# Kernel tuning notes

Measured on AMD Instinct MI355X. Metric: run time of the kernel, lower is better.

The kernel has to match this reference:

```python
import jax, jax.numpy as jnp
import numpy as np

N = 100000
K = 20
SCALES = (5, 10, 20)
D = 256  # dimoffeat


def _leaky(x):
    return jax.nn.leaky_relu(x, negative_slope=0.2)


def setup_inputs() -> dict:
    key = jax.random.key(0)
    ks = jax.random.split(key, 20)
    S = len(SCALES)
    inp = {
        "points": jax.random.normal(ks[0], (N, 3), dtype=jnp.float32),
        "neighbor_indices": jax.random.randint(ks[1], (N, K), 0, N, dtype=jnp.int64),
        # per-scale patch PointNet weights, stacked over the 3 scales
        "pw1": jax.random.normal(ks[2], (S, D // 4, 3), dtype=jnp.float32) * 0.05,
        "pb1": jax.random.normal(ks[3], (S, D // 4), dtype=jnp.float32) * 0.05,
        "pw2": jax.random.normal(ks[4], (S, D // 2, D // 4), dtype=jnp.float32) * 0.05,
        "pb2": jax.random.normal(ks[5], (S, D // 2), dtype=jnp.float32) * 0.05,
        "pw3": jax.random.normal(ks[6], (S, D, D // 2), dtype=jnp.float32) * 0.05,
        "pb3": jax.random.normal(ks[7], (S, D), dtype=jnp.float32) * 0.05,
        # shared MLP (all 1x1 convs == linears)
        "sw1": jax.random.normal(ks[8], (D, S * D), dtype=jnp.float32) * 0.05,
        "sb1": jax.random.normal(ks[9], (D,), dtype=jnp.float32) * 0.05,
        "sw2": jax.random.normal(ks[10], (D // 2, D), dtype=jnp.float32) * 0.05,
        "sb2": jax.random.normal(ks[11], (D // 2,), dtype=jnp.float32) * 0.05,
        "sw3": jax.random.normal(ks[12], (D // 4, D // 2), dtype=jnp.float32) * 0.05,
        "sb3": jax.random.normal(ks[13], (D // 4,), dtype=jnp.float32) * 0.05,
        "sw4": jax.random.normal(ks[14], (D // 8, D // 4), dtype=jnp.float32) * 0.05,
        "sb4": jax.random.normal(ks[15], (D // 8,), dtype=jnp.float32) * 0.05,
        "sw5": jax.random.normal(ks[16], (1, D // 8), dtype=jnp.float32) * 0.05,
        "sb5": jax.random.normal(ks[17], (1,), dtype=jnp.float32) * 0.05,
    }
    return inp


def reference(points, pw1, pb1, pw2, pb2, pw3, pb3,
              sw1, sb1, sw2, sb2, sw3, sb3, sw4, sb4, sw5, sb5,
              neighbor_indices):
    feats_list = []
    for i, s in enumerate(SCALES):
        # gather neighbors and center: [N, s, 3]
        nb = points[neighbor_indices[:, :s]] - points[:, None, :]
        # 1x1-conv MLP == per-point linear layers
        h = _leaky(jnp.einsum('nsc,dc->nsd', nb, pw1[i]) + pb1[i])
        h = _leaky(jnp.einsum('nsc,dc->nsd', h, pw2[i]) + pb2[i])
        h = jnp.einsum('nsc,dc->nsd', h, pw3[i]) + pb3[i]
        feats_list.append(jnp.max(h, axis=1))  # max-pool over neighbors -> [N, D]
    x = jnp.concatenate(feats_list, axis=1)  # [N, 3*D]
    h = _leaky(x @ sw1.T + sb1)
    h = _leaky(h @ sw2.T + sb2)
    h = _leaky(h @ sw3.T + sb3)
    h = _leaky(h @ sw4.T + sb4)
    out = h @ sw5.T + sb5  # [N, 1]
    return out[:, 0]
```

## Files before the change

### kernel.cpp

```cpp
#include <hip/hip_runtime.h>


typedef _Float16 f16x8 __attribute__((ext_vector_type(8)));
typedef float f32x4 __attribute__((ext_vector_type(4)));

#define NPTS 100000
#define PPB 32
#define KMAX 20

#define PW2OFF 0
#define PW3OFF 24576
#define SW1OFF 122880
#define SW2OFF 319488
#define SW3OFF 352256
#define SW4OFF 360448
#define NFRAGS 708
#define PW1PAD_BYTES 724992

__device__ __forceinline__ float leaky(float x) { return fmaxf(x, 0.2f * x); }

struct PrepRegion { const float* src; int inC; int Kk; int fEnd; int dstOff; };
struct PrepParams {
    PrepRegion r[10];
    const float* pw1; const float* pb1;
    float* pw1pad; _Float16* dst;
};

__global__ __launch_bounds__(256) void prep_kernel(PrepParams pp) {
    int gid = blockIdx.x * 256 + threadIdx.x;
    if (gid < NFRAGS * 64) {
        int f = gid >> 6, L = gid & 63;
        int ri = 0;
        while (f >= pp.r[ri].fEnd) ri++;
        int f0 = (ri == 0) ? 0 : pp.r[ri - 1].fEnd;
        const PrepRegion R = pp.r[ri];
        int fl = f - f0;
        int nt = fl / R.Kk, kk = fl - nt * R.Kk;
        int row = nt * 16 + (L & 15);
        int col = kk * 32 + (L >> 4) * 8;
        const float* s = R.src + row * R.inC + col;
        f16x8 v;
#pragma unroll
        for (int j = 0; j < 8; ++j) v[j] = (_Float16)s[j];
        *(f16x8*)(pp.dst + R.dstOff + fl * 512 + L * 8) = v;
    } else if (gid < NFRAGS * 64 + 192) {
        int t = gid - NFRAGS * 64;
        int i = t >> 6, fd = t & 63;
        float4 w;
        w.x = pp.pw1[i * 192 + fd * 3 + 0];
        w.y = pp.pw1[i * 192 + fd * 3 + 1];
        w.z = pp.pw1[i * 192 + fd * 3 + 2];
        w.w = pp.pb1[i * 64 + fd];
        ((float4*)pp.pw1pad)[i * 64 + fd] = w;
    }
}

struct MainParams {
    const float* points; const int* nidx;
    const float* pb2; const float* pb3;
    const float* sb1; const float* sb2; const float* sb3; const float* sb4;
    const float* sw5; const float* sb5;
    const _Float16* wsH; const float* pw1pad;
    float* out;
    int n;
};

#define LDS_BYTES 41472

__global__ __launch_bounds__(256, 2) void msp_mfma(MainParams p) {
    __shared__ __align__(16) unsigned char pool[LDS_BYTES];
    float*     nbf  = (float*)pool;
    float*     pw1s = (float*)(pool + 10240);
    _Float16*  h1   = (_Float16*)(pool + 11264);
    _Float16*  h2   = (_Float16*)(pool + 15872);
    _Float16*  xi   = (_Float16*)(pool + 24576);

    const int tid  = threadIdx.x;
    const int wave = tid >> 6, lane = tid & 63;
    const int q = lane >> 4, m16 = lane & 15;
    const int n0 = blockIdx.x * PPB;

    for (int r = tid; r < PPB * KMAX; r += 256) {
        int pp_ = r & 31, k = r >> 5;
        int idx = p.nidx[(n0 + pp_) * KMAX + k];
        const float* npt = p.points + idx * 3;
        const float* cpt = p.points + (n0 + pp_) * 3;
        float4 v;
        v.x = npt[0] - cpt[0];
        v.y = npt[1] - cpt[1];
        v.z = npt[2] - cpt[2];
        v.w = 1.0f;
        ((float4*)nbf)[r] = v;
    }

    f32x4 accC[2][4];
#pragma unroll
    for (int mt = 0; mt < 2; ++mt)
#pragma unroll
        for (int t = 0; t < 4; ++t) accC[mt][t] = (f32x4){0.f, 0.f, 0.f, 0.f};

    __syncthreads();

    const int SS[3] = {5, 10, 20};
    for (int i = 0; i < 3; ++i) {
        const int S = SS[i];
        if (tid < 64)
            ((float4*)pw1s)[tid] = ((const float4*)p.pw1pad)[i * 64 + tid];

        f16x8 W2f[2][2], W3f[4][4];
#pragma unroll
        for (int t2 = 0; t2 < 2; ++t2)
#pragma unroll
            for (int kk = 0; kk < 2; ++kk)
                W2f[t2][kk] = *(const f16x8*)(p.wsH + PW2OFF +
                    (i * 16 + (2 * wave + t2) * 2 + kk) * 512 + lane * 8);
#pragma unroll
        for (int t3 = 0; t3 < 4; ++t3)
#pragma unroll
            for (int kk = 0; kk < 4; ++kk)
                W3f[t3][kk] = *(const f16x8*)(p.wsH + PW3OFF +
                    (i * 64 + (4 * wave + t3) * 4 + kk) * 512 + lane * 8);

        float b2v[2], b3v[4];
#pragma unroll
        for (int t2 = 0; t2 < 2; ++t2) b2v[t2] = p.pb2[i * 128 + (2 * wave + t2) * 16 + m16];
#pragma unroll
        for (int t3 = 0; t3 < 4; ++t3) b3v[t3] = p.pb3[i * 256 + (4 * wave + t3) * 16 + m16];

        f32x4 maxC[2][4];
#pragma unroll
        for (int mt = 0; mt < 2; ++mt)
#pragma unroll
            for (int t3 = 0; t3 < 4; ++t3)
                maxC[mt][t3] = (f32x4){-3.0e38f, -3.0e38f, -3.0e38f, -3.0e38f};

        __syncthreads();

        for (int k = 0; k < S; ++k) {
            {
                int row = tid & 31, g = tid >> 5;
                float4 nv = ((const float4*)nbf)[k * 32 + row];
                f16x8 hv;
#pragma unroll
                for (int j = 0; j < 8; ++j) {
                    float4 w = ((const float4*)pw1s)[g * 8 + j];
                    float v = fmaf(nv.x, w.x, fmaf(nv.y, w.y, fmaf(nv.z, w.z, w.w)));
                    hv[j] = (_Float16)leaky(v);
                }
                *(f16x8*)(h1 + row * 72 + g * 8) = hv;
            }
            __syncthreads();

#pragma unroll
            for (int mt = 0; mt < 2; ++mt) {
                const _Float16* ar = h1 + (mt * 16 + m16) * 72 + q * 8;
                f16x8 a0 = *(const f16x8*)(ar);
                f16x8 a1 = *(const f16x8*)(ar + 32);
                f32x4 acc[2];
#pragma unroll
                for (int t2 = 0; t2 < 2; ++t2) {
                    acc[t2] = __builtin_amdgcn_mfma_f32_16x16x32_f16(a0, W2f[t2][0],
                              (f32x4){0.f, 0.f, 0.f, 0.f}, 0, 0, 0);
                }
#pragma unroll
                for (int t2 = 0; t2 < 2; ++t2)
                    acc[t2] = __builtin_amdgcn_mfma_f32_16x16x32_f16(a1, W2f[t2][1], acc[t2], 0, 0, 0);
#pragma unroll
                for (int t2 = 0; t2 < 2; ++t2) {
                    int colb = (2 * wave + t2) * 16 + m16;
#pragma unroll
                    for (int r = 0; r < 4; ++r) {
                        float v = leaky(acc[t2][r] + b2v[t2]);
                        h2[(mt * 16 + q * 4 + r) * 136 + colb] = (_Float16)v;
                    }
                }
            }
            __syncthreads();

#pragma unroll
            for (int mt = 0; mt < 2; ++mt) {
                const _Float16* ar = h2 + (mt * 16 + m16) * 136;
                f16x8 a[4];
#pragma unroll
                for (int kk = 0; kk < 4; ++kk)
                    a[kk] = *(const f16x8*)(ar + kk * 32 + q * 8);
                f32x4 acc[4];
#pragma unroll
                for (int t3 = 0; t3 < 4; ++t3)
                    acc[t3] = __builtin_amdgcn_mfma_f32_16x16x32_f16(a[0], W3f[t3][0],
                              (f32x4){0.f, 0.f, 0.f, 0.f}, 0, 0, 0);
#pragma unroll
                for (int kk = 1; kk < 4; ++kk)
#pragma unroll
                    for (int t3 = 0; t3 < 4; ++t3)
                        acc[t3] = __builtin_amdgcn_mfma_f32_16x16x32_f16(a[kk], W3f[t3][kk], acc[t3], 0, 0, 0);
#pragma unroll
                for (int t3 = 0; t3 < 4; ++t3)
#pragma unroll
                    for (int r = 0; r < 4; ++r)
                        maxC[mt][t3][r] = fmaxf(maxC[mt][t3][r], acc[t3][r]);
            }
        }

#pragma unroll
        for (int mt = 0; mt < 2; ++mt)
#pragma unroll
            for (int t3 = 0; t3 < 4; ++t3) {
                int col = (4 * wave + t3) * 16 + m16;
#pragma unroll
                for (int r = 0; r < 4; ++r)
                    xi[(mt * 16 + q * 4 + r) * 264 + col] = (_Float16)(maxC[mt][t3][r] + b3v[t3]);
            }
        __syncthreads();

#pragma unroll
        for (int mt = 0; mt < 2; ++mt) {
            const _Float16* ar = xi + (mt * 16 + m16) * 264;
            f16x8 a[8];
#pragma unroll
            for (int kk = 0; kk < 8; ++kk)
                a[kk] = *(const f16x8*)(ar + kk * 32 + q * 8);
#pragma unroll
            for (int kk = 0; kk < 8; ++kk)
#pragma unroll
                for (int t = 0; t < 4; ++t) {
                    int nt = 4 * wave + t;
                    f16x8 b = *(const f16x8*)(p.wsH + SW1OFF +
                        (nt * 24 + i * 8 + kk) * 512 + lane * 8);
                    accC[mt][t] = __builtin_amdgcn_mfma_f32_16x16x32_f16(a[kk], b, accC[mt][t], 0, 0, 0);
                }
        }
        __syncthreads();
    }

#pragma unroll
    for (int mt = 0; mt < 2; ++mt)
#pragma unroll
        for (int t = 0; t < 4; ++t) {
            int col = (4 * wave + t) * 16 + m16;
            float b = p.sb1[col];
#pragma unroll
            for (int r = 0; r < 4; ++r)
                xi[(mt * 16 + q * 4 + r) * 264 + col] = (_Float16)leaky(accC[mt][t][r] + b);
        }
    __syncthreads();

#pragma unroll
    for (int mt = 0; mt < 2; ++mt) {
        const _Float16* ar = xi + (mt * 16 + m16) * 264;
        f16x8 a[8];
#pragma unroll
        for (int kk = 0; kk < 8; ++kk)
            a[kk] = *(const f16x8*)(ar + kk * 32 + q * 8);
        f32x4 acc[2];
        acc[0] = acc[1] = (f32x4){0.f, 0.f, 0.f, 0.f};
#pragma unroll
        for (int kk = 0; kk < 8; ++kk)
#pragma unroll
            for (int t2 = 0; t2 < 2; ++t2) {
                int nt = 2 * wave + t2;
                f16x8 b = *(const f16x8*)(p.wsH + SW2OFF + (nt * 8 + kk) * 512 + lane * 8);
                acc[t2] = __builtin_amdgcn_mfma_f32_16x16x32_f16(a[kk], b, acc[t2], 0, 0, 0);
            }
#pragma unroll
        for (int t2 = 0; t2 < 2; ++t2) {
            int col = (2 * wave + t2) * 16 + m16;
            float b = p.sb2[col];
#pragma unroll
            for (int r = 0; r < 4; ++r)
                h2[(mt * 16 + q * 4 + r) * 136 + col] = (_Float16)leaky(acc[t2][r] + b);
        }
    }
    __syncthreads();

    {
        f16x8 a[2][4];
#pragma unroll
        for (int mt = 0; mt < 2; ++mt) {
            const _Float16* ar = h2 + (mt * 16 + m16) * 136;
#pragma unroll
            for (int kk = 0; kk < 4; ++kk)
                a[mt][kk] = *(const f16x8*)(ar + kk * 32 + q * 8);
        }
        f32x4 acc[2];
        acc[0] = acc[1] = (f32x4){0.f, 0.f, 0.f, 0.f};
#pragma unroll
        for (int kk = 0; kk < 4; ++kk) {
            f16x8 b = *(const f16x8*)(p.wsH + SW3OFF + (wave * 4 + kk) * 512 + lane * 8);
#pragma unroll
            for (int mt = 0; mt < 2; ++mt)
                acc[mt] = __builtin_amdgcn_mfma_f32_16x16x32_f16(a[mt][kk], b, acc[mt], 0, 0, 0);
        }
        int col = wave * 16 + m16;
        float bb = p.sb3[col];
#pragma unroll
        for (int mt = 0; mt < 2; ++mt)
#pragma unroll
            for (int r = 0; r < 4; ++r)
                h1[(mt * 16 + q * 4 + r) * 72 + col] = (_Float16)leaky(acc[mt][r] + bb);
    }
    __syncthreads();

    if (wave < 2) {
#pragma unroll
        for (int mt = 0; mt < 2; ++mt) {
            const _Float16* ar = h1 + (mt * 16 + m16) * 72;
            f16x8 a0 = *(const f16x8*)(ar + q * 8);
            f16x8 a1 = *(const f16x8*)(ar + 32 + q * 8);
            f32x4 acc = __builtin_amdgcn_mfma_f32_16x16x32_f16(a0,
                *(const f16x8*)(p.wsH + SW4OFF + (wave * 2 + 0) * 512 + lane * 8),
                (f32x4){0.f, 0.f, 0.f, 0.f}, 0, 0, 0);
            acc = __builtin_amdgcn_mfma_f32_16x16x32_f16(a1,
                *(const f16x8*)(p.wsH + SW4OFF + (wave * 2 + 1) * 512 + lane * 8),
                acc, 0, 0, 0);
            int col = wave * 16 + m16;
            float b = p.sb4[col];
#pragma unroll
            for (int r = 0; r < 4; ++r)
                nbf[(mt * 16 + q * 4 + r) * 33 + col] = leaky(acc[r] + b);
        }
    }
    __syncthreads();

    if (tid < PPB) {
        float acc = p.sb5[0];
#pragma unroll
        for (int c = 0; c < 32; ++c)
            acc = fmaf(nbf[tid * 33 + c], p.sw5[c], acc);
        p.out[n0 + tid] = acc;
    }
}

extern "C" void kernel_launch(void* const* d_in, const int* in_sizes, int n_in,
                              void* d_out, int out_size, void* d_ws, size_t ws_size,
                              hipStream_t stream) {
    const float* points = (const float*)d_in[0];
    const int*   nidx   = (const int*)d_in[1];
    const float* pw1 = (const float*)d_in[2];  const float* pb1 = (const float*)d_in[3];
    const float* pw2 = (const float*)d_in[4];  const float* pb2 = (const float*)d_in[5];
    const float* pw3 = (const float*)d_in[6];  const float* pb3 = (const float*)d_in[7];
    const float* sw1 = (const float*)d_in[8];  const float* sb1 = (const float*)d_in[9];
    const float* sw2 = (const float*)d_in[10]; const float* sb2 = (const float*)d_in[11];
    const float* sw3 = (const float*)d_in[12]; const float* sb3 = (const float*)d_in[13];
    const float* sw4 = (const float*)d_in[14]; const float* sb4 = (const float*)d_in[15];
    const float* sw5 = (const float*)d_in[16]; const float* sb5 = (const float*)d_in[17];

    _Float16* wsH = (_Float16*)d_ws;
    float* pw1pad = (float*)((char*)d_ws + PW1PAD_BYTES);

    PrepParams pp;
    for (int i = 0; i < 3; ++i)
        pp.r[i] = { pw2 + i * 8192, 64, 2, 16 * (i + 1), PW2OFF + i * 8192 };
    for (int i = 0; i < 3; ++i)
        pp.r[3 + i] = { pw3 + i * 32768, 128, 4, 48 + 64 * (i + 1), PW3OFF + i * 32768 };
    pp.r[6] = { sw1, 768, 24, 624, SW1OFF };
    pp.r[7] = { sw2, 256, 8, 688, SW2OFF };
    pp.r[8] = { sw3, 128, 4, 704, SW3OFF };
    pp.r[9] = { sw4, 64, 2, 708, SW4OFF };
    pp.pw1 = pw1; pp.pb1 = pb1;
    pp.pw1pad = pw1pad; pp.dst = wsH;

    int prep_threads = NFRAGS * 64 + 192;
    hipLaunchKernelGGL(prep_kernel, dim3((prep_threads + 255) / 256), dim3(256), 0, stream, pp);

    MainParams mp;
    mp.points = points; mp.nidx = nidx;
    mp.pb2 = pb2; mp.pb3 = pb3;
    mp.sb1 = sb1; mp.sb2 = sb2; mp.sb3 = sb3; mp.sb4 = sb4;
    mp.sw5 = sw5; mp.sb5 = sb5;
    mp.wsH = wsH; mp.pw1pad = pw1pad;
    mp.out = (float*)d_out;
    mp.n = in_sizes[0] / 3;

    int blocks = mp.n / PPB;
    hipLaunchKernelGGL(msp_mfma, dim3(blocks), dim3(256), 0, stream, mp);
}
```

Before: 502.2 us.

## Batch five neighbors per MFMA pass with transposed operands and folded biases

The patch-MLP loop now processes chunks of five neighbors at once (160 rows), so one barrier pair covers five neighbors instead of one and there are fewer synchronisations per scale. MFMA operands are swapped so weights are the A operand and activations the B operand, which allows packed f16x4 vector stores to LDS and bias loading as the accumulator init. Layer-1 weights move from LDS into registers, and bias plus leaky for layer 2 are done in packed half precision with round-toward-zero conversion. LDS use nearly doubles to 76.8KB, which may reduce occupancy, and the half-precision activation adds small rounding differences.

New measurement: 517.5 us. +3.1%, slower.

```diff
diff --git a/kernel.cpp b/kernel.cpp
--- a/kernel.cpp
+++ b/kernel.cpp
@@ -2,9 +2,10 @@
 
 
 typedef _Float16 f16x8 __attribute__((ext_vector_type(8)));
-typedef float f32x4 __attribute__((ext_vector_type(4)));
-
-#define NPTS 100000
+typedef _Float16 f16x4 __attribute__((ext_vector_type(4)));
+typedef __fp16   h16x2 __attribute__((ext_vector_type(2)));
+typedef float    f32x4 __attribute__((ext_vector_type(4)));
+
 #define PPB 32
 #define KMAX 20
 
@@ -17,7 +18,41 @@
 #define NFRAGS 708
 #define PW1PAD_BYTES 724992
 
-__device__ __forceinline__ float leaky(float x) { return fmaxf(x, 0.2f * x); }
+#define NB_OFF 0
+#define H1_OFF 10240
+#define H2_OFF 33280
+#define LDS_BYTES 76800
+#define H1S 72
+#define H2S 136
+#define XIS 264
+#define X2S 264
+#define H3S 136
+#define H4S 72
+#define O4S 36
+
+__device__ __forceinline__ float leakyf(float x) { return fmaxf(x, 0.2f * x); }
+
+__device__ __forceinline__ f16x4 pkrtz4(f32x4 a) {
+    h16x2 lo = __builtin_amdgcn_cvt_pkrtz(a[0], a[1]);
+    h16x2 hi = __builtin_amdgcn_cvt_pkrtz(a[2], a[3]);
+    f16x4 r;
+    r[0] = (_Float16)lo[0]; r[1] = (_Float16)lo[1];
+    r[2] = (_Float16)hi[0]; r[3] = (_Float16)hi[1];
+    return r;
+}
+__device__ __forceinline__ f16x4 leaky4h(f16x4 h) {
+    f16x4 s = h * (_Float16)0.2f;
+    return __builtin_elementwise_max(h, s);
+}
+__device__ __forceinline__ f16x4 rne4(f32x4 a) {
+    f16x4 r; r[0] = (_Float16)a[0]; r[1] = (_Float16)a[1];
+    r[2] = (_Float16)a[2]; r[3] = (_Float16)a[3];
+    return r;
+}
+__device__ __forceinline__ f32x4 ldbias4(const float* b) {
+    float4 t = *(const float4*)b;
+    return (f32x4){t.x, t.y, t.z, t.w};
+}
 
 struct PrepRegion { const float* src; int inC; int Kk; int fEnd; int dstOff; };
 struct PrepParams {
@@ -65,15 +100,16 @@
     int n;
 };
 
-#define LDS_BYTES 41472
-
 __global__ __launch_bounds__(256, 2) void msp_mfma(MainParams p) {
     __shared__ __align__(16) unsigned char pool[LDS_BYTES];
-    float*     nbf  = (float*)pool;
-    float*     pw1s = (float*)(pool + 10240);
-    _Float16*  h1   = (_Float16*)(pool + 11264);
-    _Float16*  h2   = (_Float16*)(pool + 15872);
-    _Float16*  xi   = (_Float16*)(pool + 24576);
+    float*    nbf = (float*)(pool + NB_OFF);
+    _Float16* h1  = (_Float16*)(pool + H1_OFF);
+    _Float16* h2  = (_Float16*)(pool + H2_OFF);
+    _Float16* xi  = (_Float16*)(pool + H2_OFF);
+    _Float16* x2  = (_Float16*)(pool + H1_OFF);
+    _Float16* h3  = (_Float16*)(pool + NB_OFF);
+    _Float16* h4  = (_Float16*)(pool + H2_OFF);
+    float*    out4= (float*)(pool + H2_OFF + 8192);
 
     const int tid  = threadIdx.x;
     const int wave = tid >> 6, lane = tid & 63;
@@ -95,229 +131,201 @@
 
     f32x4 accC[2][4];
 #pragma unroll
-    for (int mt = 0; mt < 2; ++mt)
-#pragma unroll
-        for (int t = 0; t < 4; ++t) accC[mt][t] = (f32x4){0.f, 0.f, 0.f, 0.f};
-
-    __syncthreads();
-
-    const int SS[3] = {5, 10, 20};
+    for (int mt = 0; mt < 4; ++mt) {
+        f32x4 b = ldbias4(p.sb1 + (wave * 4 + mt) * 16 + q * 4);
+        accC[0][mt] = b; accC[1][mt] = b;
+    }
+    __syncthreads();
+
+    const int NC[3] = {1, 2, 4};
     for (int i = 0; i < 3; ++i) {
-        const int S = SS[i];
-        if (tid < 64)
-            ((float4*)pw1s)[tid] = ((const float4*)p.pw1pad)[i * 64 + tid];
-
         f16x8 W2f[2][2], W3f[4][4];
 #pragma unroll
-        for (int t2 = 0; t2 < 2; ++t2)
+        for (int mt = 0; mt < 2; ++mt)
 #pragma unroll
             for (int kk = 0; kk < 2; ++kk)
-                W2f[t2][kk] = *(const f16x8*)(p.wsH + PW2OFF +
-                    (i * 16 + (2 * wave + t2) * 2 + kk) * 512 + lane * 8);
-#pragma unroll
-        for (int t3 = 0; t3 < 4; ++t3)
+                W2f[mt][kk] = *(const f16x8*)(p.wsH + PW2OFF +
+                    (i * 16 + (wave * 2 + mt) * 2 + kk) * 512 + lane * 8);
+#pragma unroll
+        for (int mt = 0; mt < 4; ++mt)
 #pragma unroll
             for (int kk = 0; kk < 4; ++kk)
-                W3f[t3][kk] = *(const f16x8*)(p.wsH + PW3OFF +
-                    (i * 64 + (4 * wave + t3) * 4 + kk) * 512 + lane * 8);
-
-        float b2v[2], b3v[4];
-#pragma unroll
-        for (int t2 = 0; t2 < 2; ++t2) b2v[t2] = p.pb2[i * 128 + (2 * wave + t2) * 16 + m16];
-#pragma unroll
-        for (int t3 = 0; t3 < 4; ++t3) b3v[t3] = p.pb3[i * 256 + (4 * wave + t3) * 16 + m16];
+                W3f[mt][kk] = *(const f16x8*)(p.wsH + PW3OFF +
+                    (i * 64 + (wave * 4 + mt) * 4 + kk) * 512 + lane * 8);
+
+        float4 w1r[8];
+        {
+            const float4* pw14 = (const float4*)p.pw1pad + i * 64 + (tid >> 5) * 8;
+#pragma unroll
+            for (int j = 0; j < 8; ++j) w1r[j] = pw14[j];
+        }
+        f32x4 b2v[2], b3v[4];
+#pragma unroll
+        for (int mt = 0; mt < 2; ++mt)
+            b2v[mt] = ldbias4(p.pb2 + i * 128 + (wave * 2 + mt) * 16 + q * 4);
+#pragma unroll
+        for (int mt = 0; mt < 4; ++mt)
+            b3v[mt] = ldbias4(p.pb3 + i * 256 + (wave * 4 + mt) * 16 + q * 4);
 
         f32x4 maxC[2][4];
 #pragma unroll
+        for (int pt = 0; pt < 2; ++pt)
+#pragma unroll
+            for (int mt = 0; mt < 4; ++mt)
+                maxC[pt][mt] = (f32x4){-3.0e38f, -3.0e38f, -3.0e38f, -3.0e38f};
+
+        for (int c = 0; c < NC[i]; ++c) {
+            const int k0 = c * 5;
+            {
+                int p_ = tid & 31, g = tid >> 5;
+                for (int kc = 0; kc < 5; ++kc) {
+                    float4 nv = ((const float4*)nbf)[(k0 + kc) * 32 + p_];
+                    f32x4 v0, v1;
+#pragma unroll
+                    for (int j = 0; j < 4; ++j) {
+                        float4 w = w1r[j];
+                        v0[j] = leakyf(fmaf(nv.x, w.x, fmaf(nv.y, w.y, fmaf(nv.z, w.z, w.w))));
+                    }
+#pragma unroll
+                    for (int j = 0; j < 4; ++j) {
+                        float4 w = w1r[4 + j];
+                        v1[j] = leakyf(fmaf(nv.x, w.x, fmaf(nv.y, w.y, fmaf(nv.z, w.z, w.w))));
+                    }
+                    f16x4 a = pkrtz4(v0), b = pkrtz4(v1);
+                    f16x8 hv;
+#pragma unroll
+                    for (int j = 0; j < 4; ++j) { hv[j] = a[j]; hv[4 + j] = b[j]; }
+                    *(f16x8*)(h1 + (kc * 32 + p_) * H1S + g * 8) = hv;
+                }
+            }
+            __syncthreads();
+
+            for (int nt = 0; nt < 10; ++nt) {
+                const _Float16* br = h1 + (nt * 16 + m16) * H1S + q * 8;
+                f16x8 b0 = *(const f16x8*)br;
+                f16x8 b1 = *(const f16x8*)(br + 32);
+                f32x4 acc0 = __builtin_amdgcn_mfma_f32_16x16x32_f16(W2f[0][0], b0, b2v[0], 0, 0, 0);
+                f32x4 acc1 = __builtin_amdgcn_mfma_f32_16x16x32_f16(W2f[1][0], b0, b2v[1], 0, 0, 0);
+                acc0 = __builtin_amdgcn_mfma_f32_16x16x32_f16(W2f[0][1], b1, acc0, 0, 0, 0);
+                acc1 = __builtin_amdgcn_mfma_f32_16x16x32_f16(W2f[1][1], b1, acc1, 0, 0, 0);
+                _Float16* wr = h2 + (nt * 16 + m16) * H2S + q * 4;
+                *(f16x4*)(wr + (wave * 2 + 0) * 16) = leaky4h(pkrtz4(acc0));
+                *(f16x4*)(wr + (wave * 2 + 1) * 16) = leaky4h(pkrtz4(acc1));
+            }
+            __syncthreads();
+
+            for (int nt = 0; nt < 10; ++nt) {
+                const _Float16* br = h2 + (nt * 16 + m16) * H2S + q * 8;
+                f16x8 b[4];
+#pragma unroll
+                for (int kk = 0; kk < 4; ++kk) b[kk] = *(const f16x8*)(br + kk * 32);
+                f32x4 acc[4];
+#pragma unroll
+                for (int mt = 0; mt < 4; ++mt)
+                    acc[mt] = __builtin_amdgcn_mfma_f32_16x16x32_f16(W3f[mt][0], b[0], b3v[mt], 0, 0, 0);
+#pragma unroll
+                for (int kk = 1; kk < 4; ++kk)
+#pragma unroll
+                    for (int mt = 0; mt < 4; ++mt)
+                        acc[mt] = __builtin_amdgcn_mfma_f32_16x16x32_f16(W3f[mt][kk], b[kk], acc[mt], 0, 0, 0);
+                int pt = nt & 1;
+#pragma unroll
+                for (int mt = 0; mt < 4; ++mt)
+                    maxC[pt][mt] = __builtin_elementwise_max(maxC[pt][mt], acc[mt]);
+            }
+        }
+
+        __syncthreads();
+#pragma unroll
+        for (int pt = 0; pt < 2; ++pt)
+#pragma unroll
+            for (int mt = 0; mt < 4; ++mt)
+                *(f16x4*)(xi + (pt * 16 + m16) * XIS + (wave * 4 + mt) * 16 + q * 4)
+                    = rne4(maxC[pt][mt]);
+        __syncthreads();
+
+        for (int nt = 0; nt < 2; ++nt) {
+            const _Float16* br = xi + (nt * 16 + m16) * XIS + q * 8;
+            f16x8 bf[8];
+#pragma unroll
+            for (int kk = 0; kk < 8; ++kk) bf[kk] = *(const f16x8*)(br + kk * 32);
+#pragma unroll
+            for (int kk = 0; kk < 8; ++kk)
+#pragma unroll
+                for (int mt = 0; mt < 4; ++mt) {
+                    f16x8 a = *(const f16x8*)(p.wsH + SW1OFF +
+                        ((wave * 4 + mt) * 24 + i * 8 + kk) * 512 + lane * 8);
+                    accC[nt][mt] = __builtin_amdgcn_mfma_f32_16x16x32_f16(a, bf[kk], accC[nt][mt], 0, 0, 0);
+                }
+        }
+    }
+
+#pragma unroll
+    for (int nt = 0; nt < 2; ++nt)
+#pragma unroll
+        for (int mt = 0; mt < 4; ++mt) {
+            f32x4 v = accC[nt][mt];
+#pragma unroll
+            for (int r = 0; r < 4; ++r) v[r] = leakyf(v[r]);
+            *(f16x4*)(x2 + (nt * 16 + m16) * X2S + (wave * 4 + mt) * 16 + q * 4) = rne4(v);
+        }
+    __syncthreads();
+
+    for (int nt = 0; nt < 2; ++nt) {
+        const _Float16* br = x2 + (nt * 16 + m16) * X2S + q * 8;
+        f16x8 bf[8];
+#pragma unroll
+        for (int kk = 0; kk < 8; ++kk) bf[kk] = *(const f16x8*)(br + kk * 32);
+        f32x4 acc[2];
+#pragma unroll
         for (int mt = 0; mt < 2; ++mt)
-#pragma unroll
-            for (int t3 = 0; t3 < 4; ++t3)
-                maxC[mt][t3] = (f32x4){-3.0e38f, -3.0e38f, -3.0e38f, -3.0e38f};
-
-        __syncthreads();
-
-        for (int k = 0; k < S; ++k) {
-            {
-                int row = tid & 31, g = tid >> 5;
-                float4 nv = ((const float4*)nbf)[k * 32 + row];
-                f16x8 hv;
-#pragma unroll
-                for (int j = 0; j < 8; ++j) {
-                    float4 w = ((const float4*)pw1s)[g * 8 + j];
-                    float v = fmaf(nv.x, w.x, fmaf(nv.y, w.y, fmaf(nv.z, w.z, w.w)));
-                    hv[j] = (_Float16)leaky(v);
-                }
-                *(f16x8*)(h1 + row * 72 + g * 8) = hv;
-            }
-            __syncthreads();
-
+            acc[mt] = ldbias4(p.sb2 + (wave * 2 + mt) * 16 + q * 4);
+#pragma unroll
+        for (int kk = 0; kk < 8; ++kk)
 #pragma unroll
             for (int mt = 0; mt < 2; ++mt) {
-                const _Float16* ar = h1 + (mt * 16 + m16) * 72 + q * 8;
-                f16x8 a0 = *(const f16x8*)(ar);
-                f16x8 a1 = *(const f16x8*)(ar + 32);
-                f32x4 acc[2];
-#pragma unroll
-                for (int t2 = 0; t2 < 2; ++t2) {
-                    acc[t2] = __builtin_amdgcn_mfma_f32_16x16x32_f16(a0, W2f[t2][0],
-                              (f32x4){0.f, 0.f, 0.f, 0.f}, 0, 0, 0);
-                }
-#pragma unroll
-                for (int t2 = 0; t2 < 2; ++t2)
-                    acc[t2] = __builtin_amdgcn_mfma_f32_16x16x32_f16(a1, W2f[t2][1], acc[t2], 0, 0, 0);
-#pragma unroll
-                for (int t2 = 0; t2 < 2; ++t2) {
-                    int colb = (2 * wave + t2) * 16 + m16;
-#pragma unroll
-                    for (int r = 0; r < 4; ++r) {
-                        float v = leaky(acc[t2][r] + b2v[t2]);
-                        h2[(mt * 16 + q * 4 + r) * 136 + colb] = (_Float16)v;
-                    }
-                }
-            }
-            __syncthreads();
-
-#pragma unroll
-            for (int mt = 0; mt < 2; ++mt) {
-                const _Float16* ar = h2 + (mt * 16 + m16) * 136;
-                f16x8 a[4];
-#pragma unroll
-                for (int kk = 0; kk < 4; ++kk)
-                    a[kk] = *(const f16x8*)(ar + kk * 32 + q * 8);
-                f32x4 acc[4];
-#pragma unroll
-                for (int t3 = 0; t3 < 4; ++t3)
-                    acc[t3] = __builtin_amdgcn_mfma_f32_16x16x32_f16(a[0], W3f[t3][0],
-                              (f32x4){0.f, 0.f, 0.f, 0.f}, 0, 0, 0);
-#pragma unroll
-                for (int kk = 1; kk < 4; ++kk)
-#pragma unroll
-                    for (int t3 = 0; t3 < 4; ++t3)
-                        acc[t3] = __builtin_amdgcn_mfma_f32_16x16x32_f16(a[kk], W3f[t3][kk], acc[t3], 0, 0, 0);
-#pragma unroll
-                for (int t3 = 0; t3 < 4; ++t3)
-#pragma unroll
-                    for (int r = 0; r < 4; ++r)
-                        maxC[mt][t3][r] = fmaxf(maxC[mt][t3][r], acc[t3][r]);
-            }
-        }
-
-#pragma unroll
-        for (int mt = 0; mt < 2; ++mt)
-#pragma unroll
-            for (int t3 = 0; t3 < 4; ++t3) {
-                int col = (4 * wave + t3) * 16 + m16;
-#pragma unroll
-                for (int r = 0; r < 4; ++r)
-                    xi[(mt * 16 + q * 4 + r) * 264 + col] = (_Float16)(maxC[mt][t3][r] + b3v[t3]);
-            }
-        __syncthreads();
-
+                f16x8 a = *(const f16x8*)(p.wsH + SW2OFF +
+                    ((wave * 2 + mt) * 8 + kk) * 512 + lane * 8);
+                acc[mt] = __builtin_amdgcn_mfma_f32_16x16x32_f16(a, bf[kk], acc[mt], 0, 0, 0);
+            }
 #pragma unroll
         for (int mt = 0; mt < 2; ++mt) {
-            const _Float16* ar = xi + (mt * 16 + m16) * 264;
-            f16x8 a[8];
-#pragma unroll
-            for (int kk = 0; kk < 8; ++kk)
-                a[kk] = *(const f16x8*)(ar + kk * 32 + q * 8);
-#pragma unroll
-            for (int kk = 0; kk < 8; ++kk)
-#pragma unroll
-                for (int t = 0; t < 4; ++t) {
-                    int nt = 4 * wave + t;
-                    f16x8 b = *(const f16x8*)(p.wsH + SW1OFF +
-                        (nt * 24 + i * 8 + kk) * 512 + lane * 8);
-                    accC[mt][t] = __builtin_amdgcn_mfma_f32_16x16x32_f16(a[kk], b, accC[mt][t], 0, 0, 0);
-                }
-        }
-        __syncthreads();
-    }
-
-#pragma unroll
-    for (int mt = 0; mt < 2; ++mt)
-#pragma unroll
-        for (int t = 0; t < 4; ++t) {
-            int col = (4 * wave + t) * 16 + m16;
-            float b = p.sb1[col];
-#pragma unroll
-            for (int r = 0; r < 4; ++r)
-                xi[(mt * 16 + q * 4 + r) * 264 + col] = (_Float16)leaky(accC[mt][t][r] + b);
-        }
-    __syncthreads();
-
-#pragma unroll
-    for (int mt = 0; mt < 2; ++mt) {
-        const _Float16* ar = xi + (mt * 16 + m16) * 264;
-        f16x8 a[8];
-#pragma unroll
-        for (int kk = 0; kk < 8; ++kk)
-            a[kk] = *(const f16x8*)(ar + kk * 32 + q * 8);
-        f32x4 acc[2];
-        acc[0] = acc[1] = (f32x4){0.f, 0.f, 0.f, 0.f};
-#pragma unroll
-        for (int kk = 0; kk < 8; ++kk)
-#pragma unroll
-            for (int t2 = 0; t2 < 2; ++t2) {
-                int nt = 2 * wave + t2;
-                f16x8 b = *(const f16x8*)(p.wsH + SW2OFF + (nt * 8 + kk) * 512 + lane * 8);
-                acc[t2] = __builtin_amdgcn_mfma_f32_16x16x32_f16(a[kk], b, acc[t2], 0, 0, 0);
-            }
-#pragma unroll
-        for (int t2 = 0; t2 < 2; ++t2) {
-            int col = (2 * wave + t2) * 16 + m16;
-            float b = p.sb2[col];
-#pragma unroll
-            for (int r = 0; r < 4; ++r)
-                h2[(mt * 16 + q * 4 + r) * 136 + col] = (_Float16)leaky(acc[t2][r] + b);
-        }
-    }
-    __syncthreads();
-
-    {
-        f16x8 a[2][4];
-#pragma unroll
-        for (int mt = 0; mt < 2; ++mt) {
-            const _Float16* ar = h2 + (mt * 16 + m16) * 136;
-#pragma unroll
-            for (int kk = 0; kk < 4; ++kk)
-                a[mt][kk] = *(const f16x8*)(ar + kk * 32 + q * 8);
-        }
-        f32x4 acc[2];
-        acc[0] = acc[1] = (f32x4){0.f, 0.f, 0.f, 0.f};
+            f32x4 v = acc[mt];
+#pragma unroll
+            for (int r = 0; r < 4; ++r) v[r] = leakyf(v[r]);
+            *(f16x4*)(h3 + (nt * 16 + m16) * H3S + (wave * 2 + mt) * 16 + q * 4) = rne4(v);
+        }
+    }
+    __syncthreads();
+
+    for (int nt = 0; nt < 2; ++nt) {
+        const _Float16* br = h3 + (nt * 16 + m16) * H3S + q * 8;
+        f32x4 acc = ldbias4(p.sb3 + wave * 16 + q * 4);
 #pragma unroll
         for (int kk = 0; kk < 4; ++kk) {
-            f16x8 b = *(const f16x8*)(p.wsH + SW3OFF + (wave * 4 + kk) * 512 + lane * 8);
-#pragma unroll
-            for (int mt = 0; mt < 2; ++mt)
-                acc[mt] = __builtin_amdgcn_mfma_f32_16x16x32_f16(a[mt][kk], b, acc[mt], 0, 0, 0);
-        }
-        int col = wave * 16 + m16;
-        float bb = p.sb3[col];
-#pragma unroll
-        for (int mt = 0; mt < 2; ++mt)
-#pragma unroll
-            for (int r = 0; r < 4; ++r)
-                h1[(mt * 16 + q * 4 + r) * 72 + col] = (_Float16)leaky(acc[mt][r] + bb);
+            f16x8 bf = *(const f16x8*)(br + kk * 32);
+            f16x8 a = *(const f16x8*)(p.wsH + SW3OFF + (wave * 4 + kk) * 512 + lane * 8);
+            acc = __builtin_amdgcn_mfma_f32_16x16x32_f16(a, bf, acc, 0, 0, 0);
+        }
+#pragma unroll
+        for (int r = 0; r < 4; ++r) acc[r] = leakyf(acc[r]);
+        *(f16x4*)(h4 + (nt * 16 + m16) * H4S + wave * 16 + q * 4) = rne4(acc);
     }
     __syncthreads();
 
     if (wave < 2) {
-#pragma unroll
-        for (int mt = 0; mt < 2; ++mt) {
-            const _Float16* ar = h1 + (mt * 16 + m16) * 72;
-            f16x8 a0 = *(const f16x8*)(ar + q * 8);
-            f16x8 a1 = *(const f16x8*)(ar + 32 + q * 8);
-            f32x4 acc = __builtin_amdgcn_mfma_f32_16x16x32_f16(a0,
-                *(const f16x8*)(p.wsH + SW4OFF + (wave * 2 + 0) * 512 + lane * 8),
-                (f32x4){0.f, 0.f, 0.f, 0.f}, 0, 0, 0);
-            acc = __builtin_amdgcn_mfma_f32_16x16x32_f16(a1,
-                *(const f16x8*)(p.wsH + SW4OFF + (wave * 2 + 1) * 512 + lane * 8),
-                acc, 0, 0, 0);
-            int col = wave * 16 + m16;
-            float b = p.sb4[col];
-#pragma unroll
-            for (int r = 0; r < 4; ++r)
-                nbf[(mt * 16 + q * 4 + r) * 33 + col] = leaky(acc[r] + b);
+        for (int nt = 0; nt < 2; ++nt) {
+            const _Float16* br = h4 + (nt * 16 + m16) * H4S + q * 8;
+            f32x4 acc = ldbias4(p.sb4 + wave * 16 + q * 4);
+#pragma unroll
+            for (int kk = 0; kk < 2; ++kk) {
+                f16x8 bf = *(const f16x8*)(br + kk * 32);
+                f16x8 a = *(const f16x8*)(p.wsH + SW4OFF + (wave * 2 + kk) * 512 + lane * 8);
+                acc = __builtin_amdgcn_mfma_f32_16x16x32_f16(a, bf, acc, 0, 0, 0);
+            }
+#pragma unroll
+            for (int r = 0; r < 4; ++r) acc[r] = leakyf(acc[r]);
+            *(f32x4*)(out4 + (nt * 16 + m16) * O4S + wave * 16 + q * 4) = acc;
         }
     }
     __syncthreads();
@@ -326,7 +334,7 @@
         float acc = p.sb5[0];
 #pragma unroll
         for (int c = 0; c < 32; ++c)
-            acc = fmaf(nbf[tid * 33 + c], p.sw5[c], acc);
+            acc = fmaf(out4[tid * O4S + c], p.sw5[c], acc);
         p.out[n0 + tid] = acc;
     }
 }
```
